# Kernel tuning notes

Measured on AMD Instinct MI355X. Metric: run time of the kernel, lower is better.

The kernel has to match this reference:

```python
import jax, jax.numpy as jnp
import numpy as np

N_NODES = 100000
N_EDGES = 1600000
IN_FEATS = 64
HIDDEN = 64
TOPO_DIM = 16
NUM_CLASSES = 4
NUM_GRAPHS = 64


def setup_inputs() -> dict:
    key = jax.random.key(0)
    ks = jax.random.split(key, 10)
    x = jax.random.normal(ks[0], (N_NODES, IN_FEATS), dtype=jnp.float32)
    edge_index = jax.random.randint(ks[1], (2, N_EDGES), 0, N_NODES, dtype=jnp.int64)
    batch = jnp.sort(jax.random.randint(ks[2], (N_NODES,), 0, NUM_GRAPHS, dtype=jnp.int64))
    topo = jax.random.normal(ks[3], (NUM_GRAPHS, TOPO_DIM), dtype=jnp.float32)
    # GCNConv weights (glorot-ish scale) and biases
    W1 = jax.random.normal(ks[4], (IN_FEATS, HIDDEN), dtype=jnp.float32) / np.sqrt(IN_FEATS)
    b1 = jnp.zeros((HIDDEN,), dtype=jnp.float32)
    W2 = jax.random.normal(ks[5], (HIDDEN, HIDDEN), dtype=jnp.float32) / np.sqrt(HIDDEN)
    b2 = jnp.zeros((HIDDEN,), dtype=jnp.float32)
    Wlin = jax.random.normal(ks[6], (HIDDEN + TOPO_DIM, NUM_CLASSES), dtype=jnp.float32) / np.sqrt(HIDDEN + TOPO_DIM)
    blin = jnp.zeros((NUM_CLASSES,), dtype=jnp.float32)
    return {"x": x, "edge_index": edge_index, "batch": batch, "topo": topo,
            "W1": W1, "b1": b1, "W2": W2, "b2": b2, "Wlin": Wlin, "blin": blin}


def _gcn_conv(x, W, b, src, dst, deg_inv_sqrt):
    # PyG GCNConv: add self-loops, symmetric normalization D^-1/2 (A+I) D^-1/2, then linear.
    xw = x @ W                                   # [N, H]
    norm = deg_inv_sqrt[src] * deg_inv_sqrt[dst]  # [E]
    msgs = xw[src] * norm[:, None]               # gather + scale, [E, H]
    agg = jax.ops.segment_sum(msgs, dst, num_segments=x.shape[0])
    # self-loop contribution: norm_ii = deg_inv_sqrt[i]^2
    agg = agg + xw * (deg_inv_sqrt * deg_inv_sqrt)[:, None]
    return agg + b


def reference(x, edge_index, batch, topo, W1, b1, W2, b2, Wlin, blin):
    src, dst = edge_index[0], edge_index[1]
    n = x.shape[0]
    # degree including self-loop
    deg = jax.ops.segment_sum(jnp.ones_like(dst, dtype=x.dtype), dst, num_segments=n) + 1.0
    deg_inv_sqrt = jax.lax.rsqrt(deg)
    h = jax.nn.relu(_gcn_conv(x, W1, b1, src, dst, deg_inv_sqrt))
    # F.dropout(p=0.5, training=False) -> identity at inference
    h = jax.nn.relu(_gcn_conv(h, W2, b2, src, dst, deg_inv_sqrt))
    # global mean pool over graphs
    sums = jax.ops.segment_sum(h, batch, num_segments=NUM_GRAPHS)
    counts = jax.ops.segment_sum(jnp.ones((n,), dtype=h.dtype), batch, num_segments=NUM_GRAPHS)
    g = sums / jnp.maximum(counts, 1.0)[:, None]  # [G, H]
    gtopo = jnp.concatenate([g, topo], axis=1)    # [G, H + topo_dim]
    return gtopo @ Wlin + blin
```

## Files before the change

### kernel.cpp

```cpp
#include <hip/hip_runtime.h>
#include <hip/hip_bf16.h>

#define NGRAPH  64
#define TOPO_D  16
#define NBLK    512
#define MAXB    512
#define GROWS   8

typedef float v2f __attribute__((ext_vector_type(2)));

static __device__ __forceinline__ unsigned f2bf(float f) {
    unsigned u = __float_as_uint(f);
    return (u + 0x7FFFu + ((u >> 16) & 1u)) >> 16;
}
static __device__ __forceinline__ float bf_lo(unsigned u) { return __uint_as_float(u << 16); }
static __device__ __forceinline__ float bf_hi(unsigned u) { return __uint_as_float(u & 0xFFFF0000u); }

static __device__ __forceinline__ void gemm_rows_bf(
        const float* __restrict__ X, const float* Wreg,
        unsigned short* __restrict__ Abf, int row0, int N, int lane) {
    #pragma unroll
    for (int j = 0; j < GROWS; ++j) {
        int row = row0 + j;
        if (row >= N) return;
        const float* xr = X + (size_t)row * 64;
        float acc = 0.0f;
        #pragma unroll
        for (int k = 0; k < 64; ++k) acc = fmaf(xr[k], Wreg[k], acc);
        Abf[(size_t)row * 64 + lane] = (unsigned short)f2bf(acc);
    }
}

__global__ __launch_bounds__(256) void hybrid_gemm_hist_kernel(
        const float* __restrict__ X, const float* __restrict__ W,
        unsigned short* __restrict__ Abf,
        const int* __restrict__ dst, int* __restrict__ bhist,
        int N, int E, int Gg, int nb2, int CE) {
    __shared__ int hist[MAXB];
    int t = threadIdx.x;
    if ((int)blockIdx.x < Gg) {
        int lane = t & 63;
        float Wreg[64];
        #pragma unroll
        for (int k = 0; k < 64; ++k) Wreg[k] = W[k * 64 + lane];
        int wave = __builtin_amdgcn_readfirstlane(blockIdx.x * 4 + (t >> 6));
        gemm_rows_bf(X, Wreg, Abf, wave * GROWS, N, lane);
    } else {
        int blk = blockIdx.x - Gg;
        for (int i = t; i < nb2; i += 256) hist[i] = 0;
        __syncthreads();
        int e0 = blk * CE, e1 = min(e0 + CE, E);
        for (int e = e0 + t; e < e1; e += 256) atomicAdd(&hist[dst[e] >> 8], 1);
        __syncthreads();
        for (int i = t; i < nb2; i += 256) bhist[blk * nb2 + i] = hist[i];
    }
}

__global__ __launch_bounds__(256) void scan_cols_kernel(
        int* __restrict__ bhist, int* __restrict__ ctot, int nb2) {
    __shared__ int sd[256];
    int c = blockIdx.x;
    int t = threadIdx.x;
    int v0 = bhist[t * nb2 + c];
    int v1 = bhist[(t + 256) * nb2 + c];
    int tsum = v0 + v1;
    sd[t] = tsum; __syncthreads();
    for (int off = 1; off < 256; off <<= 1) {
        int u = (t >= off) ? sd[t - off] : 0;
        __syncthreads();
        sd[t] += u;
        __syncthreads();
    }
    int excl = sd[t] - tsum;
    bhist[t * nb2 + c] = excl;
    bhist[(t + 256) * nb2 + c] = excl + v0;
    if (t == 255) ctot[c] = sd[255];
}

__global__ void scan_gstart_kernel(const int* __restrict__ ctot, int* __restrict__ cbase,
                                   const int* __restrict__ batch, int* __restrict__ gstart,
                                   float* __restrict__ gsum, int nb2, int N) {
    if (blockIdx.x == 0) {
        int lane = threadIdx.x;
        if (lane >= 64) return;
        int base = lane * 8;
        int vals[8];
        int s = 0;
        #pragma unroll
        for (int k = 0; k < 8; ++k) {
            int i = base + k;
            int v = (i < nb2) ? ctot[i] : 0;
            vals[k] = s; s += v;
        }
        int inc = s;
        for (int off = 1; off < 64; off <<= 1) {
            int u = __shfl_up(inc, off, 64);
            if (lane >= off) inc += u;
        }
        int lexcl = inc - s;
        #pragma unroll
        for (int k = 0; k < 8; ++k) {
            int i = base + k;
            if (i <= nb2) cbase[i] = lexcl + vals[k];
        }
    } else if (blockIdx.x == 1) {
        int g = threadIdx.x;
        if (g > NGRAPH) return;
        int lo = 0, hi = N;
        while (lo < hi) {
            int mid = (lo + hi) >> 1;
            if (batch[mid] < g) lo = mid + 1; else hi = mid;
        }
        gstart[g] = lo;
    } else {
        for (int i = threadIdx.x; i < NGRAPH * 64; i += 256) gsum[i] = 0.f;
    }
}

__global__ __launch_bounds__(256) void scatter_sorted_kernel(
        const int* __restrict__ src, const int* __restrict__ dst,
        const int* __restrict__ bhist, const int* __restrict__ cbase,
        unsigned* __restrict__ ebuf, int E, int nb2, int CE) {
    __shared__ int cur[MAXB];
    int blk = blockIdx.x, t = threadIdx.x;
    for (int i = t; i < nb2; i += 256) cur[i] = bhist[blk * nb2 + i] + cbase[i];
    __syncthreads();
    int e0 = blk * CE, e1 = min(e0 + CE, E);
    for (int e = e0 + t; e < e1; e += 256) {
        int d = dst[e];
        int pos = atomicAdd(&cur[d >> 8], 1);
        ebuf[pos] = ((unsigned)src[e] << 8) | (unsigned)(d & 255);
    }
}

__global__ __launch_bounds__(256) void build_csr_kernel(
        const unsigned* __restrict__ ebuf, const int* __restrict__ cbase,
        int* __restrict__ col, int* __restrict__ rowptr,
        int* __restrict__ degi, float* __restrict__ dis,
        const unsigned* __restrict__ Abf32, unsigned* __restrict__ A8, int N) {
    __shared__ int cnt[256];
    __shared__ int loff[256];
    __shared__ float disS[256];
    int b = blockIdx.x, t = threadIdx.x;
    int e0 = cbase[b], e1 = cbase[b + 1];
    cnt[t] = 0; __syncthreads();
    for (int i = e0 + t; i < e1; i += 256) atomicAdd(&cnt[ebuf[i] & 255u], 1);
    __syncthreads();
    int v = cnt[t];
    loff[t] = v; __syncthreads();
    for (int off = 1; off < 256; off <<= 1) {
        int u = (t >= off) ? loff[t - off] : 0;
        __syncthreads();
        loff[t] += u;
        __syncthreads();
    }
    int excl = loff[t] - v;
    int node = b * 256 + t;
    float ds = rsqrtf((float)v + 1.0f);
    disS[t] = ds;
    if (node < N) {
        degi[node]   = v;
        dis[node]    = ds;
        rowptr[node] = e0 + excl;
    }
    __syncthreads();
    cnt[t] = excl;
    __syncthreads();
    for (int i = e0 + t; i < e1; i += 256) {
        unsigned p = ebuf[i];
        int pos = atomicAdd(&cnt[p & 255u], 1);
        col[e0 + pos] = (int)(p >> 8);
    }
    int base8 = b * 256 * 16;
    for (int i = t; i < 256 * 16; i += 256) {
        int r = i >> 4;
        int dwo = i & 15;
        int nd = b * 256 + r;
        if (nd < N) {
            float d2 = disS[r];
            unsigned u0 = Abf32[(size_t)nd * 32 + dwo * 2];
            unsigned u1 = Abf32[(size_t)nd * 32 + dwo * 2 + 1];
            int dw = __builtin_amdgcn_cvt_pk_fp8_f32(bf_lo(u0) * d2, bf_hi(u0) * d2, 0, false);
            dw = __builtin_amdgcn_cvt_pk_fp8_f32(bf_lo(u1) * d2, bf_hi(u1) * d2, dw, true);
            A8[base8 + i] = (unsigned)dw;
        }
    }
}

static __device__ __forceinline__ void gather_node(
        const unsigned* __restrict__ A8, const int* __restrict__ col,
        int beg, int deg, int node, int f8, float acc[8]) {
    const char* Abase = (const char*)A8 + f8 * 8;
    uint2 an = *(const uint2*)(Abase + ((size_t)node << 6));
    v2f a0 = __builtin_amdgcn_cvt_pk_f32_fp8(an.x, false);
    v2f a1 = __builtin_amdgcn_cvt_pk_f32_fp8(an.x, true);
    v2f a2 = __builtin_amdgcn_cvt_pk_f32_fp8(an.y, false);
    v2f a3 = __builtin_amdgcn_cvt_pk_f32_fp8(an.y, true);
    acc[0] = a0.x; acc[1] = a0.y; acc[2] = a1.x; acc[3] = a1.y;
    acc[4] = a2.x; acc[5] = a2.y; acc[6] = a3.x; acc[7] = a3.y;
    int j = 0;
    for (; j + 4 <= deg; j += 4) {
        int s0 = col[beg + j]     << 6;
        int s1 = col[beg + j + 1] << 6;
        int s2 = col[beg + j + 2] << 6;
        int s3 = col[beg + j + 3] << 6;
        uint2 v0 = *(const uint2*)(Abase + s0);
        uint2 v1 = *(const uint2*)(Abase + s1);
        uint2 v2 = *(const uint2*)(Abase + s2);
        uint2 v3 = *(const uint2*)(Abase + s3);
        v2f f0, f1, f2, f3;
        f0 = __builtin_amdgcn_cvt_pk_f32_fp8(v0.x, false); acc[0] += f0.x; acc[1] += f0.y;
        f1 = __builtin_amdgcn_cvt_pk_f32_fp8(v0.x, true);  acc[2] += f1.x; acc[3] += f1.y;
        f2 = __builtin_amdgcn_cvt_pk_f32_fp8(v0.y, false); acc[4] += f2.x; acc[5] += f2.y;
        f3 = __builtin_amdgcn_cvt_pk_f32_fp8(v0.y, true);  acc[6] += f3.x; acc[7] += f3.y;
        f0 = __builtin_amdgcn_cvt_pk_f32_fp8(v1.x, false); acc[0] += f0.x; acc[1] += f0.y;
        f1 = __builtin_amdgcn_cvt_pk_f32_fp8(v1.x, true);  acc[2] += f1.x; acc[3] += f1.y;
        f2 = __builtin_amdgcn_cvt_pk_f32_fp8(v1.y, false); acc[4] += f2.x; acc[5] += f2.y;
        f3 = __builtin_amdgcn_cvt_pk_f32_fp8(v1.y, true);  acc[6] += f3.x; acc[7] += f3.y;
        f0 = __builtin_amdgcn_cvt_pk_f32_fp8(v2.x, false); acc[0] += f0.x; acc[1] += f0.y;
        f1 = __builtin_amdgcn_cvt_pk_f32_fp8(v2.x, true);  acc[2] += f1.x; acc[3] += f1.y;
        f2 = __builtin_amdgcn_cvt_pk_f32_fp8(v2.y, false); acc[4] += f2.x; acc[5] += f2.y;
        f3 = __builtin_amdgcn_cvt_pk_f32_fp8(v2.y, true);  acc[6] += f3.x; acc[7] += f3.y;
        f0 = __builtin_amdgcn_cvt_pk_f32_fp8(v3.x, false); acc[0] += f0.x; acc[1] += f0.y;
        f1 = __builtin_amdgcn_cvt_pk_f32_fp8(v3.x, true);  acc[2] += f1.x; acc[3] += f1.y;
        f2 = __builtin_amdgcn_cvt_pk_f32_fp8(v3.y, false); acc[4] += f2.x; acc[5] += f2.y;
        f3 = __builtin_amdgcn_cvt_pk_f32_fp8(v3.y, true);  acc[6] += f3.x; acc[7] += f3.y;
    }
    for (; j < deg; ++j) {
        int s = col[beg + j] << 6;
        uint2 v = *(const uint2*)(Abase + s);
        v2f f0 = __builtin_amdgcn_cvt_pk_f32_fp8(v.x, false);
        v2f f1 = __builtin_amdgcn_cvt_pk_f32_fp8(v.x, true);
        v2f f2 = __builtin_amdgcn_cvt_pk_f32_fp8(v.y, false);
        v2f f3 = __builtin_amdgcn_cvt_pk_f32_fp8(v.y, true);
        acc[0] += f0.x; acc[1] += f0.y; acc[2] += f1.x; acc[3] += f1.y;
        acc[4] += f2.x; acc[5] += f2.y; acc[6] += f3.x; acc[7] += f3.y;
    }
}

__global__ __launch_bounds__(256) void pull_csr_kernel(
        const unsigned* __restrict__ A8, unsigned* __restrict__ C8,
        const int* __restrict__ rowptr, const int* __restrict__ degi,
        const float* __restrict__ dis, const float* __restrict__ bias,
        const int* __restrict__ col, int N) {
    int wave = (blockIdx.x * blockDim.x + threadIdx.x) >> 6;
    int lane = threadIdx.x & 63;
    int i = lane >> 3;
    int f8 = lane & 7;
    int node = wave * 8 + i;
    bool valid = node < N;
    if (!valid) node = N - 1;
    int deg = degi[node];
    int beg = rowptr[node];
    float acc[8];
    gather_node(A8, col, beg, deg, node, f8, acc);
    float d = dis[node];
    float4 b0 = ((const float4*)bias)[f8 * 2];
    float4 b1 = ((const float4*)bias)[f8 * 2 + 1];
    float r0 = fmaxf(d * acc[0] + b0.x, 0.f);
    float r1 = fmaxf(d * acc[1] + b0.y, 0.f);
    float r2 = fmaxf(d * acc[2] + b0.z, 0.f);
    float r3 = fmaxf(d * acc[3] + b0.w, 0.f);
    float r4 = fmaxf(d * acc[4] + b1.x, 0.f);
    float r5 = fmaxf(d * acc[5] + b1.y, 0.f);
    float r6 = fmaxf(d * acc[6] + b1.z, 0.f);
    float r7 = fmaxf(d * acc[7] + b1.w, 0.f);
    if (valid) {
        int p0 = __builtin_amdgcn_cvt_pk_fp8_f32(d * r0, d * r1, 0, false);
        p0 = __builtin_amdgcn_cvt_pk_fp8_f32(d * r2, d * r3, p0, true);
        int p1 = __builtin_amdgcn_cvt_pk_fp8_f32(d * r4, d * r5, 0, false);
        p1 = __builtin_amdgcn_cvt_pk_fp8_f32(d * r6, d * r7, p1, true);
        uint2 o; o.x = (unsigned)p0; o.y = (unsigned)p1;
        *(uint2*)((char*)C8 + ((size_t)node << 6) + (f8 << 3)) = o;
    }
}

__global__ __launch_bounds__(256) void pull2_pool_kernel(
        const unsigned* __restrict__ C8, const int* __restrict__ rowptr,
        const int* __restrict__ degi, const float* __restrict__ dis,
        const float* __restrict__ bias, const int* __restrict__ col,
        const int* __restrict__ batch, const float* __restrict__ W2,
        float* __restrict__ gsum, int N) {
    __shared__ float w2s[4096];
    __shared__ float sred[32][72];
    __shared__ float red[4][65];
    int t = threadIdx.x;
    ((float4*)w2s)[t]       = ((const float4*)W2)[t];
    ((float4*)w2s)[t + 256] = ((const float4*)W2)[t + 256];
    ((float4*)w2s)[t + 512] = ((const float4*)W2)[t + 512];
    ((float4*)w2s)[t + 768] = ((const float4*)W2)[t + 768];
    int wave = (blockIdx.x * blockDim.x + t) >> 6;
    int lane = t & 63;
    int w = t >> 6;
    int i = lane >> 3;
    int f8 = lane & 7;
    int node = wave * 8 + i;
    bool valid = node < N;
    if (!valid) node = N - 1;
    int deg = degi[node];
    int beg = rowptr[node];
    float acc[8];
    gather_node(C8, col, beg, deg, node, f8, acc);
    float* sp = &sred[w * 8 + i][f8 * 8];
    sp[0] = acc[0]; sp[1] = acc[1]; sp[2] = acc[2]; sp[3] = acc[3];
    sp[4] = acc[4]; sp[5] = acc[5]; sp[6] = acc[6]; sp[7] = acc[7];
    __syncthreads();
    float g0 = 0.f, g1 = 0.f, g2 = 0.f, g3 = 0.f, g4 = 0.f, g5 = 0.f, g6 = 0.f, g7 = 0.f;
    #pragma unroll
    for (int kc = 0; kc < 16; ++kc) {
        float wa = w2s[(kc * 4 + 0) * 64 + lane];
        float wb = w2s[(kc * 4 + 1) * 64 + lane];
        float wc = w2s[(kc * 4 + 2) * 64 + lane];
        float wd = w2s[(kc * 4 + 3) * 64 + lane];
        float4 sv;
        sv = *(const float4*)&sred[w * 8 + 0][kc * 4];
        g0 = fmaf(sv.x, wa, fmaf(sv.y, wb, fmaf(sv.z, wc, fmaf(sv.w, wd, g0))));
        sv = *(const float4*)&sred[w * 8 + 1][kc * 4];
        g1 = fmaf(sv.x, wa, fmaf(sv.y, wb, fmaf(sv.z, wc, fmaf(sv.w, wd, g1))));
        sv = *(const float4*)&sred[w * 8 + 2][kc * 4];
        g2 = fmaf(sv.x, wa, fmaf(sv.y, wb, fmaf(sv.z, wc, fmaf(sv.w, wd, g2))));
        sv = *(const float4*)&sred[w * 8 + 3][kc * 4];
        g3 = fmaf(sv.x, wa, fmaf(sv.y, wb, fmaf(sv.z, wc, fmaf(sv.w, wd, g3))));
        sv = *(const float4*)&sred[w * 8 + 4][kc * 4];
        g4 = fmaf(sv.x, wa, fmaf(sv.y, wb, fmaf(sv.z, wc, fmaf(sv.w, wd, g4))));
        sv = *(const float4*)&sred[w * 8 + 5][kc * 4];
        g5 = fmaf(sv.x, wa, fmaf(sv.y, wb, fmaf(sv.z, wc, fmaf(sv.w, wd, g5))));
        sv = *(const float4*)&sred[w * 8 + 6][kc * 4];
        g6 = fmaf(sv.x, wa, fmaf(sv.y, wb, fmaf(sv.z, wc, fmaf(sv.w, wd, g6))));
        sv = *(const float4*)&sred[w * 8 + 7][kc * 4];
        g7 = fmaf(sv.x, wa, fmaf(sv.y, wb, fmaf(sv.z, wc, fmaf(sv.w, wd, g7))));
    }
    int base = (blockIdx.x * 4 + w) * 8;
    float d0 = dis[min(base + 0, N - 1)];
    float d1 = dis[min(base + 1, N - 1)];
    float d2 = dis[min(base + 2, N - 1)];
    float d3 = dis[min(base + 3, N - 1)];
    float d4 = dis[min(base + 4, N - 1)];
    float d5 = dis[min(base + 5, N - 1)];
    float d6 = dis[min(base + 6, N - 1)];
    float d7 = dis[min(base + 7, N - 1)];
    float bf = bias[lane];
    float h0 = fmaxf(fmaf(d0, g0, bf), 0.f);
    float h1 = fmaxf(fmaf(d1, g1, bf), 0.f);
    float h2 = fmaxf(fmaf(d2, g2, bf), 0.f);
    float h3 = fmaxf(fmaf(d3, g3, bf), 0.f);
    float h4 = fmaxf(fmaf(d4, g4, bf), 0.f);
    float h5 = fmaxf(fmaf(d5, g5, bf), 0.f);
    float h6 = fmaxf(fmaf(d6, g6, bf), 0.f);
    float h7 = fmaxf(fmaf(d7, g7, bf), 0.f);
    if (base + 0 >= N) h0 = 0.f;
    if (base + 1 >= N) h1 = 0.f;
    if (base + 2 >= N) h2 = 0.f;
    if (base + 3 >= N) h3 = 0.f;
    if (base + 4 >= N) h4 = 0.f;
    if (base + 5 >= N) h5 = 0.f;
    if (base + 6 >= N) h6 = 0.f;
    if (base + 7 >= N) h7 = 0.f;
    int nodeA = blockIdx.x * 32;
    int gA = batch[min(nodeA, N - 1)];
    int gB = batch[min(nodeA + 31, N - 1)];
    if (gA == gB) {
        red[w][lane] = h0 + h1 + h2 + h3 + h4 + h5 + h6 + h7;
        __syncthreads();
        if (t < 64) {
            float s = red[0][t] + red[1][t] + red[2][t] + red[3][t];
            unsafeAtomicAdd(&gsum[gA * 64 + t], s);
        }
    } else {
        int q0 = batch[min(base + 0, N - 1)]; unsafeAtomicAdd(&gsum[q0 * 64 + lane], h0);
        int q1 = batch[min(base + 1, N - 1)]; unsafeAtomicAdd(&gsum[q1 * 64 + lane], h1);
        int q2 = batch[min(base + 2, N - 1)]; unsafeAtomicAdd(&gsum[q2 * 64 + lane], h2);
        int q3 = batch[min(base + 3, N - 1)]; unsafeAtomicAdd(&gsum[q3 * 64 + lane], h3);
        int q4 = batch[min(base + 4, N - 1)]; unsafeAtomicAdd(&gsum[q4 * 64 + lane], h4);
        int q5 = batch[min(base + 5, N - 1)]; unsafeAtomicAdd(&gsum[q5 * 64 + lane], h5);
        int q6 = batch[min(base + 6, N - 1)]; unsafeAtomicAdd(&gsum[q6 * 64 + lane], h6);
        int q7 = batch[min(base + 7, N - 1)]; unsafeAtomicAdd(&gsum[q7 * 64 + lane], h7);
    }
}

__global__ __launch_bounds__(256) void head_kernel(
        const float* __restrict__ gsum, const int* __restrict__ gstart,
        const float* __restrict__ topo, const float* __restrict__ Wlin,
        const float* __restrict__ blin, float* __restrict__ out) {
    int t = threadIdx.x;
    int g = t >> 2;
    int c = t & 3;
    float cntf = (float)(gstart[g + 1] - gstart[g]);
    float inv = 1.0f / fmaxf(cntf, 1.0f);
    float v = blin[c];
    #pragma unroll
    for (int f = 0; f < 64; ++f) v += gsum[g * 64 + f] * inv * Wlin[f * 4 + c];
    #pragma unroll
    for (int t2 = 0; t2 < TOPO_D; ++t2) v += topo[g * TOPO_D + t2] * Wlin[(64 + t2) * 4 + c];
    out[g * 4 + c] = v;
}

extern "C" void kernel_launch(void* const* d_in, const int* in_sizes, int n_in,
                              void* d_out, int out_size, void* d_ws, size_t ws_size,
                              hipStream_t stream) {
    const float* x     = (const float*)d_in[0];
    const int*   ei    = (const int*)d_in[1];
    const int*   batch = (const int*)d_in[2];
    const float* topo  = (const float*)d_in[3];
    const float* W1    = (const float*)d_in[4];
    const float* b1    = (const float*)d_in[5];
    const float* W2    = (const float*)d_in[6];
    const float* b2    = (const float*)d_in[7];
    const float* Wlin  = (const float*)d_in[8];
    const float* blin  = (const float*)d_in[9];
    float* out = (float*)d_out;

    const int N = in_sizes[0] / 64;
    const int E = in_sizes[1] / 2;
    const int* src = ei;
    const int* dst = ei + E;
    const int nb2 = (N + 255) / 256;
    const int CE  = (E + NBLK - 1) / NBLK;

    char* ws = (char*)d_ws;
    size_t off = 0;
    unsigned short* Abf = (unsigned short*)(ws + off); off += (size_t)N * 64 * 2;
    unsigned* A8     = (unsigned*)(ws + off); off += (size_t)N * 64;
    unsigned* C8     = (unsigned*)(ws + off); off += (size_t)N * 64;
    int*      col    = (int*)     (ws + off); off += (size_t)E * 4;
    unsigned* ebuf   = (unsigned*)(ws + off); off += (size_t)E * 4;
    int*      bhist  = (int*)     (ws + off); off += (size_t)NBLK * nb2 * 4;
    int*      ctot   = (int*)     (ws + off); off += (size_t)(nb2 + 8) * 4;
    int*      cbase  = (int*)     (ws + off); off += (size_t)(nb2 + 8) * 4;
    int*      rowptr = (int*)     (ws + off); off += (size_t)(N + 1) * 4;
    int*      degi   = (int*)     (ws + off); off += (size_t)N * 4;
    float*    dis    = (float*)   (ws + off); off += (size_t)N * 4;
    int*      gstart = (int*)     (ws + off); off += (size_t)(NGRAPH + 8) * 4;
    float*    gsum   = (float*)   (ws + off); off += (size_t)NGRAPH * 64 * 4;

    const int nWaves = (N + GROWS - 1) / GROWS;
    const int Gg = (nWaves + 3) / 4;
    hybrid_gemm_hist_kernel<<<Gg + NBLK, 256, 0, stream>>>(x, W1, Abf, dst, bhist, N, E, Gg, nb2, CE);
    scan_cols_kernel<<<nb2, 256, 0, stream>>>(bhist, ctot, nb2);
    scan_gstart_kernel<<<3, 256, 0, stream>>>(ctot, cbase, batch, gstart, gsum, nb2, N);
    scatter_sorted_kernel<<<NBLK, 256, 0, stream>>>(src, dst, bhist, cbase, ebuf, E, nb2, CE);
    build_csr_kernel<<<nb2, 256, 0, stream>>>(ebuf, cbase, col, rowptr, degi, dis,
                                              (const unsigned*)Abf, A8, N);

    int pullBlocks = ((N + 7) / 8 + 3) / 4;
    pull_csr_kernel<<<pullBlocks, 256, 0, stream>>>(A8, C8, rowptr, degi, dis, b1, col, N);

    pull2_pool_kernel<<<pullBlocks, 256, 0, stream>>>(C8, rowptr, degi, dis, b2, col,
                                                      batch, W2, gsum, N);

    head_kernel<<<1, 256, 0, stream>>>(gsum, gstart, topo, Wlin, blin, out);
}
```

Measured before the change: 215.9 us.

## Remove scan_gstart kernel by fusing its work and unroll gather by eight

The small scan_gstart launch is removed. Its batch binary search and gsum zeroing move into two extra blocks of the first hybrid kernel, and the column-total prefix scan is recomputed redundantly inside each scatter block and each CSR-build block. This cuts one dependent launch and its sync gap from the serial chain, at the cost of some repeated scan work per block. The fp8 gather loop also gains an 8-way unrolled stage so more independent loads are in flight.

```diff
diff --git a/kernel.cpp b/kernel.cpp
--- a/kernel.cpp
+++ b/kernel.cpp
@@ -35,6 +35,8 @@
         const float* __restrict__ X, const float* __restrict__ W,
         unsigned short* __restrict__ Abf,
         const int* __restrict__ dst, int* __restrict__ bhist,
+        const int* __restrict__ batch, int* __restrict__ gstart,
+        float* __restrict__ gsum,
         int N, int E, int Gg, int nb2, int CE) {
     __shared__ int hist[MAXB];
     int t = threadIdx.x;
@@ -45,7 +47,7 @@
         for (int k = 0; k < 64; ++k) Wreg[k] = W[k * 64 + lane];
         int wave = __builtin_amdgcn_readfirstlane(blockIdx.x * 4 + (t >> 6));
         gemm_rows_bf(X, Wreg, Abf, wave * GROWS, N, lane);
-    } else {
+    } else if ((int)blockIdx.x < Gg + NBLK) {
         int blk = blockIdx.x - Gg;
         for (int i = t; i < nb2; i += 256) hist[i] = 0;
         __syncthreads();
@@ -53,6 +55,18 @@
         for (int e = e0 + t; e < e1; e += 256) atomicAdd(&hist[dst[e] >> 8], 1);
         __syncthreads();
         for (int i = t; i < nb2; i += 256) bhist[blk * nb2 + i] = hist[i];
+    } else if ((int)blockIdx.x == Gg + NBLK) {
+        int g = t;
+        if (g <= NGRAPH) {
+            int lo = 0, hi = N;
+            while (lo < hi) {
+                int mid = (lo + hi) >> 1;
+                if (batch[mid] < g) lo = mid + 1; else hi = mid;
+            }
+            gstart[g] = lo;
+        }
+    } else {
+        for (int i = t; i < NGRAPH * 64; i += 256) gsum[i] = 0.f;
     }
 }
 
@@ -77,53 +91,26 @@
     if (t == 255) ctot[c] = sd[255];
 }
 
-__global__ void scan_gstart_kernel(const int* __restrict__ ctot, int* __restrict__ cbase,
-                                   const int* __restrict__ batch, int* __restrict__ gstart,
-                                   float* __restrict__ gsum, int nb2, int N) {
-    if (blockIdx.x == 0) {
-        int lane = threadIdx.x;
-        if (lane >= 64) return;
-        int base = lane * 8;
-        int vals[8];
-        int s = 0;
-        #pragma unroll
-        for (int k = 0; k < 8; ++k) {
-            int i = base + k;
-            int v = (i < nb2) ? ctot[i] : 0;
-            vals[k] = s; s += v;
-        }
-        int inc = s;
-        for (int off = 1; off < 64; off <<= 1) {
-            int u = __shfl_up(inc, off, 64);
-            if (lane >= off) inc += u;
-        }
-        int lexcl = inc - s;
-        #pragma unroll
-        for (int k = 0; k < 8; ++k) {
-            int i = base + k;
-            if (i <= nb2) cbase[i] = lexcl + vals[k];
-        }
-    } else if (blockIdx.x == 1) {
-        int g = threadIdx.x;
-        if (g > NGRAPH) return;
-        int lo = 0, hi = N;
-        while (lo < hi) {
-            int mid = (lo + hi) >> 1;
-            if (batch[mid] < g) lo = mid + 1; else hi = mid;
-        }
-        gstart[g] = lo;
-    } else {
-        for (int i = threadIdx.x; i < NGRAPH * 64; i += 256) gsum[i] = 0.f;
-    }
-}
-
 __global__ __launch_bounds__(256) void scatter_sorted_kernel(
         const int* __restrict__ src, const int* __restrict__ dst,
-        const int* __restrict__ bhist, const int* __restrict__ cbase,
+        const int* __restrict__ bhist, const int* __restrict__ ctot,
         unsigned* __restrict__ ebuf, int E, int nb2, int CE) {
+    __shared__ int sd[256];
     __shared__ int cur[MAXB];
     int blk = blockIdx.x, t = threadIdx.x;
-    for (int i = t; i < nb2; i += 256) cur[i] = bhist[blk * nb2 + i] + cbase[i];
+    int v0 = (t < nb2) ? ctot[t] : 0;
+    int v1 = (t + 256 < nb2) ? ctot[t + 256] : 0;
+    int tsum = v0 + v1;
+    sd[t] = tsum; __syncthreads();
+    for (int off = 1; off < 256; off <<= 1) {
+        int u = (t >= off) ? sd[t - off] : 0;
+        __syncthreads();
+        sd[t] += u;
+        __syncthreads();
+    }
+    int excl = sd[t] - tsum;
+    if (t < nb2)       cur[t]       = bhist[blk * nb2 + t] + excl;
+    if (t + 256 < nb2) cur[t + 256] = bhist[blk * nb2 + t + 256] + excl + v0;
     __syncthreads();
     int e0 = blk * CE, e1 = min(e0 + CE, E);
     for (int e = e0 + t; e < e1; e += 256) {
@@ -134,15 +121,24 @@
 }
 
 __global__ __launch_bounds__(256) void build_csr_kernel(
-        const unsigned* __restrict__ ebuf, const int* __restrict__ cbase,
+        const unsigned* __restrict__ ebuf, const int* __restrict__ ctot,
         int* __restrict__ col, int* __restrict__ rowptr,
         int* __restrict__ degi, float* __restrict__ dis,
         const unsigned* __restrict__ Abf32, unsigned* __restrict__ A8, int N) {
     __shared__ int cnt[256];
     __shared__ int loff[256];
     __shared__ float disS[256];
+    __shared__ int redS[256];
     int b = blockIdx.x, t = threadIdx.x;
-    int e0 = cbase[b], e1 = cbase[b + 1];
+    int part = 0;
+    for (int i = t; i < b; i += 256) part += ctot[i];
+    redS[t] = part; __syncthreads();
+    for (int off = 128; off > 0; off >>= 1) {
+        if (t < off) redS[t] += redS[t + off];
+        __syncthreads();
+    }
+    int e0 = redS[0];
+    int e1 = e0 + ctot[b];
     cnt[t] = 0; __syncthreads();
     for (int i = e0 + t; i < e1; i += 256) atomicAdd(&cnt[ebuf[i] & 255u], 1);
     __syncthreads();
@@ -187,6 +183,13 @@
     }
 }
 
+#define CVT_ACC(vv) do { \
+    v2f f0_ = __builtin_amdgcn_cvt_pk_f32_fp8((vv).x, false); acc[0] += f0_.x; acc[1] += f0_.y; \
+    v2f f1_ = __builtin_amdgcn_cvt_pk_f32_fp8((vv).x, true);  acc[2] += f1_.x; acc[3] += f1_.y; \
+    v2f f2_ = __builtin_amdgcn_cvt_pk_f32_fp8((vv).y, false); acc[4] += f2_.x; acc[5] += f2_.y; \
+    v2f f3_ = __builtin_amdgcn_cvt_pk_f32_fp8((vv).y, true);  acc[6] += f3_.x; acc[7] += f3_.y; \
+} while (0)
+
 static __device__ __forceinline__ void gather_node(
         const unsigned* __restrict__ A8, const int* __restrict__ col,
         int beg, int deg, int node, int f8, float acc[8]) {
@@ -199,6 +202,26 @@
     acc[0] = a0.x; acc[1] = a0.y; acc[2] = a1.x; acc[3] = a1.y;
     acc[4] = a2.x; acc[5] = a2.y; acc[6] = a3.x; acc[7] = a3.y;
     int j = 0;
+    for (; j + 8 <= deg; j += 8) {
+        int s0 = col[beg + j]     << 6;
+        int s1 = col[beg + j + 1] << 6;
+        int s2 = col[beg + j + 2] << 6;
+        int s3 = col[beg + j + 3] << 6;
+        int s4 = col[beg + j + 4] << 6;
+        int s5 = col[beg + j + 5] << 6;
+        int s6 = col[beg + j + 6] << 6;
+        int s7 = col[beg + j + 7] << 6;
+        uint2 v0 = *(const uint2*)(Abase + s0);
+        uint2 v1 = *(const uint2*)(Abase + s1);
+        uint2 v2 = *(const uint2*)(Abase + s2);
+        uint2 v3 = *(const uint2*)(Abase + s3);
+        uint2 v4 = *(const uint2*)(Abase + s4);
+        uint2 v5 = *(const uint2*)(Abase + s5);
+        uint2 v6 = *(const uint2*)(Abase + s6);
+        uint2 v7 = *(const uint2*)(Abase + s7);
+        CVT_ACC(v0); CVT_ACC(v1); CVT_ACC(v2); CVT_ACC(v3);
+        CVT_ACC(v4); CVT_ACC(v5); CVT_ACC(v6); CVT_ACC(v7);
+    }
     for (; j + 4 <= deg; j += 4) {
         int s0 = col[beg + j]     << 6;
         int s1 = col[beg + j + 1] << 6;
@@ -208,33 +231,12 @@
         uint2 v1 = *(const uint2*)(Abase + s1);
         uint2 v2 = *(const uint2*)(Abase + s2);
         uint2 v3 = *(const uint2*)(Abase + s3);
-        v2f f0, f1, f2, f3;
-        f0 = __builtin_amdgcn_cvt_pk_f32_fp8(v0.x, false); acc[0] += f0.x; acc[1] += f0.y;
-        f1 = __builtin_amdgcn_cvt_pk_f32_fp8(v0.x, true);  acc[2] += f1.x; acc[3] += f1.y;
-        f2 = __builtin_amdgcn_cvt_pk_f32_fp8(v0.y, false); acc[4] += f2.x; acc[5] += f2.y;
-        f3 = __builtin_amdgcn_cvt_pk_f32_fp8(v0.y, true);  acc[6] += f3.x; acc[7] += f3.y;
-        f0 = __builtin_amdgcn_cvt_pk_f32_fp8(v1.x, false); acc[0] += f0.x; acc[1] += f0.y;
-        f1 = __builtin_amdgcn_cvt_pk_f32_fp8(v1.x, true);  acc[2] += f1.x; acc[3] += f1.y;
-        f2 = __builtin_amdgcn_cvt_pk_f32_fp8(v1.y, false); acc[4] += f2.x; acc[5] += f2.y;
-        f3 = __builtin_amdgcn_cvt_pk_f32_fp8(v1.y, true);  acc[6] += f3.x; acc[7] += f3.y;
-        f0 = __builtin_amdgcn_cvt_pk_f32_fp8(v2.x, false); acc[0] += f0.x; acc[1] += f0.y;
-        f1 = __builtin_amdgcn_cvt_pk_f32_fp8(v2.x, true);  acc[2] += f1.x; acc[3] += f1.y;
-        f2 = __builtin_amdgcn_cvt_pk_f32_fp8(v2.y, false); acc[4] += f2.x; acc[5] += f2.y;
-        f3 = __builtin_amdgcn_cvt_pk_f32_fp8(v2.y, true);  acc[6] += f3.x; acc[7] += f3.y;
-        f0 = __builtin_amdgcn_cvt_pk_f32_fp8(v3.x, false); acc[0] += f0.x; acc[1] += f0.y;
-        f1 = __builtin_amdgcn_cvt_pk_f32_fp8(v3.x, true);  acc[2] += f1.x; acc[3] += f1.y;
-        f2 = __builtin_amdgcn_cvt_pk_f32_fp8(v3.y, false); acc[4] += f2.x; acc[5] += f2.y;
-        f3 = __builtin_amdgcn_cvt_pk_f32_fp8(v3.y, true);  acc[6] += f3.x; acc[7] += f3.y;
+        CVT_ACC(v0); CVT_ACC(v1); CVT_ACC(v2); CVT_ACC(v3);
     }
     for (; j < deg; ++j) {
         int s = col[beg + j] << 6;
         uint2 v = *(const uint2*)(Abase + s);
-        v2f f0 = __builtin_amdgcn_cvt_pk_f32_fp8(v.x, false);
-        v2f f1 = __builtin_amdgcn_cvt_pk_f32_fp8(v.x, true);
-        v2f f2 = __builtin_amdgcn_cvt_pk_f32_fp8(v.y, false);
-        v2f f3 = __builtin_amdgcn_cvt_pk_f32_fp8(v.y, true);
-        acc[0] += f0.x; acc[1] += f0.y; acc[2] += f1.x; acc[3] += f1.y;
-        acc[4] += f2.x; acc[5] += f2.y; acc[6] += f3.x; acc[7] += f3.y;
+        CVT_ACC(v);
     }
 }
 
@@ -426,7 +428,6 @@
     unsigned* ebuf   = (unsigned*)(ws + off); off += (size_t)E * 4;
     int*      bhist  = (int*)     (ws + off); off += (size_t)NBLK * nb2 * 4;
     int*      ctot   = (int*)     (ws + off); off += (size_t)(nb2 + 8) * 4;
-    int*      cbase  = (int*)     (ws + off); off += (size_t)(nb2 + 8) * 4;
     int*      rowptr = (int*)     (ws + off); off += (size_t)(N + 1) * 4;
     int*      degi   = (int*)     (ws + off); off += (size_t)N * 4;
     float*    dis    = (float*)   (ws + off); off += (size_t)N * 4;
@@ -435,11 +436,11 @@
 
     const int nWaves = (N + GROWS - 1) / GROWS;
     const int Gg = (nWaves + 3) / 4;
-    hybrid_gemm_hist_kernel<<<Gg + NBLK, 256, 0, stream>>>(x, W1, Abf, dst, bhist, N, E, Gg, nb2, CE);
+    hybrid_gemm_hist_kernel<<<Gg + NBLK + 2, 256, 0, stream>>>(
+        x, W1, Abf, dst, bhist, batch, gstart, gsum, N, E, Gg, nb2, CE);
     scan_cols_kernel<<<nb2, 256, 0, stream>>>(bhist, ctot, nb2);
-    scan_gstart_kernel<<<3, 256, 0, stream>>>(ctot, cbase, batch, gstart, gsum, nb2, N);
-    scatter_sorted_kernel<<<NBLK, 256, 0, stream>>>(src, dst, bhist, cbase, ebuf, E, nb2, CE);
-    build_csr_kernel<<<nb2, 256, 0, stream>>>(ebuf, cbase, col, rowptr, degi, dis,
+    scatter_sorted_kernel<<<NBLK, 256, 0, stream>>>(src, dst, bhist, ctot, ebuf, E, nb2, CE);
+    build_csr_kernel<<<nb2, 256, 0, stream>>>(ebuf, ctot, col, rowptr, degi, dis,
                                               (const unsigned*)Abf, A8, N);
 
     int pullBlocks = ((N + 7) / 8 + 3) / 4;
```

Measured after the change: 213.2 us. No clear change (-1.3%).
